# Kernel optimization log

Hardware: AMD Instinct MI355X
Metric: run time of the kernel (lower is better)

Reference implementation:

```python
import jax, jax.numpy as jnp
import numpy as np

N = 100000      # num_nodes
E = 1600000     # num_edges
IN_DIM = 6
EDGE_DIM = 2
H = 5           # heads
C = 5           # out_channels per head (hidden_dim)
D = H * C       # 25, hidden width
L = 3           # num_layers
INV_SQRT_C = np.float32(1.0 / np.sqrt(C))


def setup_inputs() -> dict:
    key = jax.random.key(0)
    ks = jax.random.split(key, 18)
    s = 0.1
    inp = {
        "x": jax.random.normal(ks[0], (N, IN_DIM), dtype=jnp.float32),
        "edge_index": jax.random.randint(ks[1], (2, E), 0, N, dtype=jnp.int64),
        "edge_attr": jax.random.normal(ks[2], (E, EDGE_DIM), dtype=jnp.float32),
        # input projection
        "Wi": jax.random.normal(ks[3], (IN_DIM, D), dtype=jnp.float32) * s,
        "bi": jnp.zeros((D,), dtype=jnp.float32),
        # per-layer TransformerConv params, stacked over layers
        "Wq": jax.random.normal(ks[4], (L, D, D), dtype=jnp.float32) * s,
        "bq": jnp.zeros((L, D), dtype=jnp.float32),
        "Wk": jax.random.normal(ks[5], (L, D, D), dtype=jnp.float32) * s,
        "bk": jnp.zeros((L, D), dtype=jnp.float32),
        "Wv": jax.random.normal(ks[6], (L, D, D), dtype=jnp.float32) * s,
        "bv": jnp.zeros((L, D), dtype=jnp.float32),
        "We": jax.random.normal(ks[7], (L, EDGE_DIM, D), dtype=jnp.float32) * s,  # lin_edge, no bias
        "Wskip": jax.random.normal(ks[8], (L, D, D), dtype=jnp.float32) * s,
        "bskip": jnp.zeros((L, D), dtype=jnp.float32),
        # output head
        "Wo": jax.random.normal(ks[9], (D, 1), dtype=jnp.float32) * s,
        "bo": jnp.zeros((1,), dtype=jnp.float32),
    }
    return inp


def _forward(x, edge_index, edge_attr, Wi, bi, Wq, bq, Wk, bk, Wv, bv, We, Wskip, bskip, Wo, bo):
    src, dst = edge_index[0], edge_index[1]
    h = x @ Wi + bi  # [N, D]
    for l in range(L):
        q = (h @ Wq[l] + bq[l]).reshape(N, H, C)
        k = (h @ Wk[l] + bk[l]).reshape(N, H, C)
        v = (h @ Wv[l] + bv[l]).reshape(N, H, C)
        e = (edge_attr @ We[l]).reshape(E, H, C)  # per-edge projection
        k_j = k[src] + e                           # [E, H, C]
        alpha = jnp.einsum('ehc,ehc->eh', q[dst], k_j) * INV_SQRT_C  # [E, H]
        # scatter-softmax over destination neighborhoods (PyG softmax)
        amax = jax.ops.segment_max(alpha, dst, num_segments=N)       # [N, H]
        ex = jnp.exp(alpha - amax[dst])
        denom = jax.ops.segment_sum(ex, dst, num_segments=N)         # [N, H]
        alpha = ex / (denom[dst] + 1e-16)
        msg = (v[src] + e) * alpha[:, :, None]                       # [E, H, C]
        out = jax.ops.segment_sum(msg, dst, num_segments=N).reshape(N, D)
        h = out + h @ Wskip[l] + bskip[l]          # root_weight skip
    return jax.nn.sigmoid(h @ Wo + bo)             # [N, 1]


def reference(x, edge_index, edge_attr, Wi, bi, Wq, bq, Wk, bk, Wv, bv, We, Wskip, bskip, Wo, bo):
    return _forward(x, edge_index, edge_attr, Wi, bi, Wq, bq, Wk, bk, Wv, bv, We, Wskip, bskip, Wo, bo)
```

## Files before the change

### kernel.cpp

```cpp
#include <hip/hip_runtime.h>
#include <hip/hip_bf16.h>
#include <math.h>

#define NN 100000
#define NE 1600000
#define IN_DIM 6
#define EDGE_DIM 2
#define HH 5
#define CC 5
#define DD 25
#define DS 32
#define QS 32
#define KVS 64
#define INV_SQRT_C 0.4472135954999579f
#define SCAN_B 256
#define NB1 ((NN + SCAN_B - 1) / SCAN_B)
#define NBUK 200
#define BUKW 500
#define CAP 10000
#define CH 8000

__device__ __forceinline__ unsigned int f2bf(float f) {
    unsigned int u = __float_as_uint(f);
    return (u + 0x7fffu + ((u >> 16) & 1u)) >> 16;
}
__device__ __forceinline__ float bflo(unsigned int u) { return __uint_as_float(u << 16); }
__device__ __forceinline__ float bfhi(unsigned int u) { return __uint_as_float(u & 0xffff0000u); }

__global__ void k_init(int* __restrict__ deg, int* __restrict__ cursor) {
    int i = blockIdx.x * 256 + threadIdx.x;
    if (i < NN) deg[i] = 0;
    if (i < NBUK) cursor[i] = i * CAP;
}

__global__ __launch_bounds__(256) void k_part(const int* __restrict__ ei,
                                              const float* __restrict__ ea,
                                              int* __restrict__ deg,
                                              int* __restrict__ cursor,
                                              uint2* __restrict__ slab) {
    __shared__ int sdst[CH];
    __shared__ int scnt[NBUK];
    __shared__ int sbase[NBUK];
    __shared__ int swp[NBUK];
    int base = blockIdx.x * CH;
    for (int i = threadIdx.x; i < NBUK; i += 256) scnt[i] = 0;
    __syncthreads();
    for (int i = threadIdx.x; i < CH; i += 256) {
        int dst = ei[NE + base + i];
        sdst[i] = dst;
        atomicAdd(&deg[dst], 1);
        atomicAdd(&scnt[dst / BUKW], 1);
    }
    __syncthreads();
    for (int i = threadIdx.x; i < NBUK; i += 256) {
        sbase[i] = atomicAdd(&cursor[i], scnt[i]);
        swp[i] = 0;
    }
    __syncthreads();
    for (int i = threadIdx.x; i < CH; i += 256) {
        int dst = sdst[i];
        int b = dst / BUKW;
        int src = ei[base + i];
        float2 eav = ((const float2*)ea)[base + i];
        int p = sbase[b] + atomicAdd(&swp[b], 1);
        uint2 r;
        r.x = (unsigned)src | ((unsigned)(dst - b * BUKW) << 17);
        r.y = f2bf(eav.x) | (f2bf(eav.y) << 16);
        slab[p] = r;
    }
}

__global__ void k_scan1(const int* __restrict__ deg, int* __restrict__ excl,
                        int* __restrict__ bsum) {
    __shared__ int s[SCAN_B];
    int i = blockIdx.x * SCAN_B + threadIdx.x;
    int v = (i < NN) ? deg[i] : 0;
    s[threadIdx.x] = v;
    __syncthreads();
    for (int off = 1; off < SCAN_B; off <<= 1) {
        int t = (threadIdx.x >= off) ? s[threadIdx.x - off] : 0;
        __syncthreads();
        s[threadIdx.x] += t;
        __syncthreads();
    }
    if (i < NN) excl[i] = s[threadIdx.x] - v;
    if (threadIdx.x == SCAN_B - 1) bsum[blockIdx.x] = s[SCAN_B - 1];
}

__global__ void k_scan2(int* __restrict__ bsum) {
    __shared__ int s[512];
    int t = threadIdx.x;
    int v = (t < NB1) ? bsum[t] : 0;
    s[t] = v;
    __syncthreads();
    for (int off = 1; off < 512; off <<= 1) {
        int u = (t >= off) ? s[t - off] : 0;
        __syncthreads();
        s[t] += u;
        __syncthreads();
    }
    if (t < NB1) bsum[t] = s[t] - v;
}

__global__ void k_scan3(const int* __restrict__ excl, const int* __restrict__ bsum,
                        int* __restrict__ rowptr) {
    int i = blockIdx.x * 256 + threadIdx.x;
    if (i < NN) rowptr[i] = excl[i] + bsum[i / SCAN_B];
    if (i == 0) rowptr[NN] = NE;
}

__global__ __launch_bounds__(256) void k_place(const int* __restrict__ cursor,
                                               const uint2* __restrict__ slab,
                                               const int* __restrict__ rowptr,
                                               uint2* __restrict__ csr) {
    __shared__ int cur[BUKW];
    int b = blockIdx.x;
    int node0 = b * BUKW;
    for (int i = threadIdx.x; i < BUKW; i += 256) cur[i] = rowptr[node0 + i];
    __syncthreads();
    int begin = b * CAP;
    int cnt = cursor[b] - begin;
    for (int i = threadIdx.x; i < cnt; i += 256) {
        uint2 r = slab[begin + i];
        int dl = (int)(r.x >> 17);
        int p = atomicAdd(&cur[dl], 1);
        uint2 o;
        o.x = r.x & 0x1FFFFu;
        o.y = r.y;
        csr[p] = o;
    }
}

__global__ void k_input_proj(const float* __restrict__ x, const float* __restrict__ Wi,
                             const float* __restrict__ bi, float* __restrict__ h) {
    __shared__ float sW[IN_DIM * DD];
    __shared__ float sb[DD];
    int t = threadIdx.x;
    if (t < IN_DIM * DD) sW[t] = Wi[t];
    if (t < DD) sb[t] = bi[t];
    __syncthreads();
    int tid = blockIdx.x * blockDim.x + t;
    int n = tid / DD, d = tid - n * DD;
    if (n >= NN) return;
    float acc = sb[d];
    const float* xr = x + n * IN_DIM;
#pragma unroll
    for (int i = 0; i < IN_DIM; i++) acc += xr[i] * sW[i * DD + d];
    h[n * DS + d] = acc;
}

__global__ void k_qkv_skip(const float* __restrict__ h,
                           const float* __restrict__ Wq, const float* __restrict__ bq,
                           const float* __restrict__ Wk, const float* __restrict__ bk,
                           const float* __restrict__ Wv, const float* __restrict__ bv,
                           const float* __restrict__ Ws, const float* __restrict__ bs,
                           __hip_bfloat16* __restrict__ q, __hip_bfloat16* __restrict__ kv,
                           float* __restrict__ hout) {
    __shared__ float sWq[DD * DD], sWk[DD * DD], sWv[DD * DD], sWs[DD * DD];
    __shared__ float sb[4 * DD];
    for (int i = threadIdx.x; i < DD * DD; i += blockDim.x) {
        sWq[i] = Wq[i]; sWk[i] = Wk[i]; sWv[i] = Wv[i]; sWs[i] = Ws[i];
    }
    if (threadIdx.x < DD) {
        sb[threadIdx.x]          = bq[threadIdx.x];
        sb[DD + threadIdx.x]     = bk[threadIdx.x];
        sb[2 * DD + threadIdx.x] = bv[threadIdx.x];
        sb[3 * DD + threadIdx.x] = bs[threadIdx.x];
    }
    __syncthreads();
    int tid = blockIdx.x * blockDim.x + threadIdx.x;
    int n = tid / DD, d = tid - n * DD;
    if (n >= NN) return;
    float aq = sb[d], ak = sb[DD + d], av = sb[2 * DD + d], asv = sb[3 * DD + d];
    const float* hr = h + (size_t)n * DS;
#pragma unroll
    for (int i = 0; i < DD; i++) {
        float hv = hr[i];
        aq  += hv * sWq[i * DD + d];
        ak  += hv * sWk[i * DD + d];
        av  += hv * sWv[i * DD + d];
        asv += hv * sWs[i * DD + d];
    }
    q[(size_t)n * QS + d] = __float2bfloat16(aq * INV_SQRT_C);
    kv[(size_t)n * KVS + d]      = __float2bfloat16(ak);
    kv[(size_t)n * KVS + 32 + d] = __float2bfloat16(av);
    hout[(size_t)n * DS + d] = asv;
}

__global__ __launch_bounds__(256) void k_edge_fused(
    const int* __restrict__ rowptr, const uint2* __restrict__ csr,
    const float* __restrict__ We, const __hip_bfloat16* __restrict__ q,
    const __hip_bfloat16* __restrict__ kv, float* __restrict__ hout) {
    __shared__ float sWe[EDGE_DIM * DD];
    if (threadIdx.x < EDGE_DIM * DD) sWe[threadIdx.x] = We[threadIdx.x];
    __syncthreads();
    int n = blockIdx.x * 32 + (threadIdx.x >> 3);
    int g = threadIdx.x & 7;
    if (n >= NN) return;
    int beg = rowptr[n], end = rowptr[n + 1];

    float qa[26];
    {
        const uint4* qr = (const uint4*)(q + (size_t)n * QS);
        uint4 q0 = qr[0], q1 = qr[1], q2 = qr[2], q3 = qr[3];
        qa[0]=bflo(q0.x); qa[1]=bfhi(q0.x); qa[2]=bflo(q0.y); qa[3]=bfhi(q0.y);
        qa[4]=bflo(q0.z); qa[5]=bfhi(q0.z); qa[6]=bflo(q0.w); qa[7]=bfhi(q0.w);
        qa[8]=bflo(q1.x); qa[9]=bfhi(q1.x); qa[10]=bflo(q1.y); qa[11]=bfhi(q1.y);
        qa[12]=bflo(q1.z); qa[13]=bfhi(q1.z); qa[14]=bflo(q1.w); qa[15]=bfhi(q1.w);
        qa[16]=bflo(q2.x); qa[17]=bfhi(q2.x); qa[18]=bflo(q2.y); qa[19]=bfhi(q2.y);
        qa[20]=bflo(q2.z); qa[21]=bfhi(q2.z); qa[22]=bflo(q2.w); qa[23]=bfhi(q2.w);
        qa[24]=bflo(q3.x);
    }
    float qwx[HH], qwy[HH];
#pragma unroll
    for (int hd = 0; hd < HH; hd++) {
        float sx = 0.0f, sy = 0.0f;
#pragma unroll
        for (int c = 0; c < CC; c++) {
            int j = hd * CC + c;
            sx += qa[j] * sWe[j];
            sy += qa[j] * sWe[DD + j];
        }
        qwx[hd] = sx; qwy[hd] = sy;
    }

    float l[HH], Sx[HH], Sy[HH], accv[DD];
#pragma unroll
    for (int hd = 0; hd < HH; hd++) { l[hd] = 0.0f; Sx[hd] = 0.0f; Sy[hd] = 0.0f; }
#pragma unroll
    for (int j = 0; j < DD; j++) accv[j] = 0.0f;

    for (int p = beg + g; p < end; p += 8) {
        uint2 rec = csr[p];
        int src = (int)rec.x;
        float eax = bflo(rec.y), eay = bfhi(rec.y);

        const uint4* kr = (const uint4*)(kv + (size_t)src * KVS);
        uint4 r0 = kr[0], r1 = kr[1], r2 = kr[2], r3 = kr[3];
        uint4 r4 = kr[4], r5 = kr[5], r6 = kr[6], r7 = kr[7];

        float kb[26];
        kb[0]=bflo(r0.x); kb[1]=bfhi(r0.x); kb[2]=bflo(r0.y); kb[3]=bfhi(r0.y);
        kb[4]=bflo(r0.z); kb[5]=bfhi(r0.z); kb[6]=bflo(r0.w); kb[7]=bfhi(r0.w);
        kb[8]=bflo(r1.x); kb[9]=bfhi(r1.x); kb[10]=bflo(r1.y); kb[11]=bfhi(r1.y);
        kb[12]=bflo(r1.z); kb[13]=bfhi(r1.z); kb[14]=bflo(r1.w); kb[15]=bfhi(r1.w);
        kb[16]=bflo(r2.x); kb[17]=bfhi(r2.x); kb[18]=bflo(r2.y); kb[19]=bfhi(r2.y);
        kb[20]=bflo(r2.z); kb[21]=bfhi(r2.z); kb[22]=bflo(r2.w); kb[23]=bfhi(r2.w);
        kb[24]=bflo(r3.x);

        float al[HH];
#pragma unroll
        for (int hd = 0; hd < HH; hd++) {
            float s = eax * qwx[hd] + eay * qwy[hd];
#pragma unroll
            for (int c = 0; c < CC; c++) {
                int j = hd * CC + c;
                s += qa[j] * kb[j];
            }
            al[hd] = __expf(s);
        }

        float vb[26];
        vb[0]=bflo(r4.x); vb[1]=bfhi(r4.x); vb[2]=bflo(r4.y); vb[3]=bfhi(r4.y);
        vb[4]=bflo(r4.z); vb[5]=bfhi(r4.z); vb[6]=bflo(r4.w); vb[7]=bfhi(r4.w);
        vb[8]=bflo(r5.x); vb[9]=bfhi(r5.x); vb[10]=bflo(r5.y); vb[11]=bfhi(r5.y);
        vb[12]=bflo(r5.z); vb[13]=bfhi(r5.z); vb[14]=bflo(r5.w); vb[15]=bfhi(r5.w);
        vb[16]=bflo(r6.x); vb[17]=bfhi(r6.x); vb[18]=bflo(r6.y); vb[19]=bfhi(r6.y);
        vb[20]=bflo(r6.z); vb[21]=bfhi(r6.z); vb[22]=bflo(r6.w); vb[23]=bfhi(r6.w);
        vb[24]=bflo(r7.x);

#pragma unroll
        for (int hd = 0; hd < HH; hd++) {
            float cf = al[hd];
            l[hd]  += cf;
            Sx[hd] += cf * eax;
            Sy[hd] += cf * eay;
#pragma unroll
            for (int c = 0; c < CC; c++) {
                int j = hd * CC + c;
                accv[j] += cf * vb[j];
            }
        }
    }

#pragma unroll
    for (int off = 1; off < 8; off <<= 1) {
#pragma unroll
        for (int hd = 0; hd < HH; hd++) {
            l[hd]  += __shfl_xor(l[hd], off, 64);
            Sx[hd] += __shfl_xor(Sx[hd], off, 64);
            Sy[hd] += __shfl_xor(Sy[hd], off, 64);
        }
#pragma unroll
        for (int j = 0; j < DD; j++) accv[j] += __shfl_xor(accv[j], off, 64);
    }

    if (g == 0) {
        float* ho = hout + (size_t)n * DS;
#pragma unroll
        for (int hd = 0; hd < HH; hd++) {
            float inv = 1.0f / (l[hd] + 1e-16f);
#pragma unroll
            for (int c = 0; c < CC; c++) {
                int j = hd * CC + c;
                ho[j] += (accv[j] + Sx[hd] * sWe[j] + Sy[hd] * sWe[DD + j]) * inv;
            }
        }
    }
}

__global__ void k_head(const float* __restrict__ h, const float* __restrict__ Wo,
                       const float* __restrict__ bo, float* __restrict__ out) {
    __shared__ float sW[DD];
    __shared__ float sb0;
    if (threadIdx.x < DD) sW[threadIdx.x] = Wo[threadIdx.x];
    if (threadIdx.x == 0) sb0 = bo[0];
    __syncthreads();
    int n = blockIdx.x * blockDim.x + threadIdx.x;
    if (n >= NN) return;
    float acc = sb0;
    const float* hr = h + (size_t)n * DS;
#pragma unroll
    for (int i = 0; i < DD; i++) acc += hr[i] * sW[i];
    out[n] = 1.0f / (1.0f + __expf(-acc));
}

extern "C" void kernel_launch(void* const* d_in, const int* in_sizes, int n_in,
                              void* d_out, int out_size, void* d_ws, size_t ws_size,
                              hipStream_t stream) {
    const float* x     = (const float*)d_in[0];
    const int*   ei    = (const int*)d_in[1];
    const float* ea    = (const float*)d_in[2];
    const float* Wi    = (const float*)d_in[3];
    const float* bi    = (const float*)d_in[4];
    const float* Wq    = (const float*)d_in[5];
    const float* bq    = (const float*)d_in[6];
    const float* Wk    = (const float*)d_in[7];
    const float* bk    = (const float*)d_in[8];
    const float* Wv    = (const float*)d_in[9];
    const float* bv    = (const float*)d_in[10];
    const float* We    = (const float*)d_in[11];
    const float* Wskip = (const float*)d_in[12];
    const float* bskip = (const float*)d_in[13];
    const float* Wo    = (const float*)d_in[14];
    const float* bo    = (const float*)d_in[15];
    float* out = (float*)d_out;
    (void)in_sizes; (void)n_in; (void)out_size; (void)ws_size;

    char* wsb = (char*)d_ws;
    size_t off = 0;
    auto alloc = [&](size_t bytes) {
        void* p = wsb + off;
        off += (bytes + 127) & ~(size_t)127;
        return p;
    };
    uint2* slab   = (uint2*)alloc((size_t)NBUK * CAP * sizeof(uint2));
    uint2* csr    = (uint2*)alloc((size_t)NE * sizeof(uint2));
    __hip_bfloat16* kvrec = (__hip_bfloat16*)alloc((size_t)NN * KVS * 2);
    __hip_bfloat16* qrec  = (__hip_bfloat16*)alloc((size_t)NN * QS * 2);
    float* hA     = (float*)alloc((size_t)NN * DS * sizeof(float));
    float* hB     = (float*)alloc((size_t)NN * DS * sizeof(float));
    int*   deg    = (int*)alloc((size_t)NN * sizeof(int));
    int*   excl   = (int*)alloc((size_t)NN * sizeof(int));
    int*   bsum   = (int*)alloc((size_t)NB1 * sizeof(int));
    int*   rowptr = (int*)alloc((size_t)(NN + 1) * sizeof(int));
    int*   cursor = (int*)alloc((size_t)NBUK * sizeof(int));

    dim3 blk(256);
    int gN  = (NN + 255) / 256;
    int gND = (NN * DD + 255) / 256;
    int gF  = NN / 32;

    k_init<<<gN, blk, 0, stream>>>(deg, cursor);
    k_part<<<NBUK, blk, 0, stream>>>(ei, ea, deg, cursor, slab);
    k_scan1<<<gN, blk, 0, stream>>>(deg, excl, bsum);
    k_scan2<<<1, dim3(512), 0, stream>>>(bsum);
    k_scan3<<<gN, blk, 0, stream>>>(excl, bsum, rowptr);
    k_place<<<NBUK, blk, 0, stream>>>(cursor, slab, rowptr, csr);

    k_input_proj<<<gND, blk, 0, stream>>>(x, Wi, bi, hA);

    float* hc = hA;
    float* hn = hB;
    for (int l = 0; l < 3; l++) {
        k_qkv_skip<<<gND, blk, 0, stream>>>(hc,
                                            Wq + (size_t)l * DD * DD, bq + (size_t)l * DD,
                                            Wk + (size_t)l * DD * DD, bk + (size_t)l * DD,
                                            Wv + (size_t)l * DD * DD, bv + (size_t)l * DD,
                                            Wskip + (size_t)l * DD * DD, bskip + (size_t)l * DD,
                                            qrec, kvrec, hn);
        k_edge_fused<<<gF, blk, 0, stream>>>(rowptr, csr,
                                             We + (size_t)l * EDGE_DIM * DD,
                                             qrec, kvrec, hn);
        float* t = hc; hc = hn; hn = t;
    }
    k_head<<<gN, blk, 0, stream>>>(hc, Wo, bo, out);
}
```

Measured before the change: 430.5 us.

## Build CSR row pointers from per-bucket histograms instead of global degree scan

```diff
diff --git a/kernel.cpp b/kernel.cpp
--- a/kernel.cpp
+++ b/kernel.cpp
@@ -13,12 +13,11 @@
 #define QS 32
 #define KVS 64
 #define INV_SQRT_C 0.4472135954999579f
-#define SCAN_B 256
-#define NB1 ((NN + SCAN_B - 1) / SCAN_B)
 #define NBUK 200
 #define BUKW 500
 #define CAP 10000
-#define CH 8000
+#define KPB 800
+#define CH (NE / KPB)
 
 __device__ __forceinline__ unsigned int f2bf(float f) {
     unsigned int u = __float_as_uint(f);
@@ -27,15 +26,13 @@
 __device__ __forceinline__ float bflo(unsigned int u) { return __uint_as_float(u << 16); }
 __device__ __forceinline__ float bfhi(unsigned int u) { return __uint_as_float(u & 0xffff0000u); }
 
-__global__ void k_init(int* __restrict__ deg, int* __restrict__ cursor) {
-    int i = blockIdx.x * 256 + threadIdx.x;
-    if (i < NN) deg[i] = 0;
+__global__ void k_init(int* __restrict__ cursor) {
+    int i = threadIdx.x;
     if (i < NBUK) cursor[i] = i * CAP;
 }
 
 __global__ __launch_bounds__(256) void k_part(const int* __restrict__ ei,
                                               const float* __restrict__ ea,
-                                              int* __restrict__ deg,
                                               int* __restrict__ cursor,
                                               uint2* __restrict__ slab) {
     __shared__ int sdst[CH];
@@ -48,7 +45,6 @@
     for (int i = threadIdx.x; i < CH; i += 256) {
         int dst = ei[NE + base + i];
         sdst[i] = dst;
-        atomicAdd(&deg[dst], 1);
         atomicAdd(&scnt[dst / BUKW], 1);
     }
     __syncthreads();
@@ -70,27 +66,45 @@
     }
 }
 
-__global__ void k_scan1(const int* __restrict__ deg, int* __restrict__ excl,
-                        int* __restrict__ bsum) {
-    __shared__ int s[SCAN_B];
-    int i = blockIdx.x * SCAN_B + threadIdx.x;
-    int v = (i < NN) ? deg[i] : 0;
-    s[threadIdx.x] = v;
-    __syncthreads();
-    for (int off = 1; off < SCAN_B; off <<= 1) {
-        int t = (threadIdx.x >= off) ? s[threadIdx.x - off] : 0;
+__global__ void k_scanB(const int* __restrict__ cursor, int* __restrict__ bucketOff,
+                        int* __restrict__ rowptr) {
+    __shared__ int s[256];
+    int t = threadIdx.x;
+    int v = (t < NBUK) ? (cursor[t] - t * CAP) : 0;
+    s[t] = v;
+    __syncthreads();
+    for (int off = 1; off < 256; off <<= 1) {
+        int u = (t >= off) ? s[t - off] : 0;
         __syncthreads();
-        s[threadIdx.x] += t;
+        s[t] += u;
         __syncthreads();
     }
-    if (i < NN) excl[i] = s[threadIdx.x] - v;
-    if (threadIdx.x == SCAN_B - 1) bsum[blockIdx.x] = s[SCAN_B - 1];
-}
-
-__global__ void k_scan2(int* __restrict__ bsum) {
+    if (t < NBUK) bucketOff[t] = s[t] - v;
+    if (t == 0) rowptr[NN] = NE;
+}
+
+__global__ __launch_bounds__(512) void k_place(const int* __restrict__ cursor,
+                                               const uint2* __restrict__ slab,
+                                               const int* __restrict__ bucketOff,
+                                               int* __restrict__ rowptr,
+                                               uint2* __restrict__ csr) {
+    __shared__ int hist[BUKW];
+    __shared__ int cur[BUKW];
     __shared__ int s[512];
+    int b = blockIdx.x;
+    int node0 = b * BUKW;
+    int begin = b * CAP;
+    int cnt = cursor[b] - begin;
+    int bOff = bucketOff[b];
+    for (int i = threadIdx.x; i < BUKW; i += 512) hist[i] = 0;
+    __syncthreads();
+    for (int i = threadIdx.x; i < cnt; i += 512) {
+        uint2 r = slab[begin + i];
+        atomicAdd(&hist[r.x >> 17], 1);
+    }
+    __syncthreads();
     int t = threadIdx.x;
-    int v = (t < NB1) ? bsum[t] : 0;
+    int v = (t < BUKW) ? hist[t] : 0;
     s[t] = v;
     __syncthreads();
     for (int off = 1; off < 512; off <<= 1) {
@@ -99,28 +113,13 @@
         s[t] += u;
         __syncthreads();
     }
-    if (t < NB1) bsum[t] = s[t] - v;
-}
-
-__global__ void k_scan3(const int* __restrict__ excl, const int* __restrict__ bsum,
-                        int* __restrict__ rowptr) {
-    int i = blockIdx.x * 256 + threadIdx.x;
-    if (i < NN) rowptr[i] = excl[i] + bsum[i / SCAN_B];
-    if (i == 0) rowptr[NN] = NE;
-}
-
-__global__ __launch_bounds__(256) void k_place(const int* __restrict__ cursor,
-                                               const uint2* __restrict__ slab,
-                                               const int* __restrict__ rowptr,
-                                               uint2* __restrict__ csr) {
-    __shared__ int cur[BUKW];
-    int b = blockIdx.x;
-    int node0 = b * BUKW;
-    for (int i = threadIdx.x; i < BUKW; i += 256) cur[i] = rowptr[node0 + i];
-    __syncthreads();
-    int begin = b * CAP;
-    int cnt = cursor[b] - begin;
-    for (int i = threadIdx.x; i < cnt; i += 256) {
+    if (t < BUKW) {
+        int o = bOff + s[t] - v;
+        rowptr[node0 + t] = o;
+        cur[t] = o;
+    }
+    __syncthreads();
+    for (int i = threadIdx.x; i < cnt; i += 512) {
         uint2 r = slab[begin + i];
         int dl = (int)(r.x >> 17);
         int p = atomicAdd(&cur[dl], 1);
@@ -360,23 +359,19 @@
     __hip_bfloat16* qrec  = (__hip_bfloat16*)alloc((size_t)NN * QS * 2);
     float* hA     = (float*)alloc((size_t)NN * DS * sizeof(float));
     float* hB     = (float*)alloc((size_t)NN * DS * sizeof(float));
-    int*   deg    = (int*)alloc((size_t)NN * sizeof(int));
-    int*   excl   = (int*)alloc((size_t)NN * sizeof(int));
-    int*   bsum   = (int*)alloc((size_t)NB1 * sizeof(int));
     int*   rowptr = (int*)alloc((size_t)(NN + 1) * sizeof(int));
     int*   cursor = (int*)alloc((size_t)NBUK * sizeof(int));
+    int*   bucketOff = (int*)alloc((size_t)NBUK * sizeof(int));
 
     dim3 blk(256);
     int gN  = (NN + 255) / 256;
     int gND = (NN * DD + 255) / 256;
     int gF  = NN / 32;
 
-    k_init<<<gN, blk, 0, stream>>>(deg, cursor);
-    k_part<<<NBUK, blk, 0, stream>>>(ei, ea, deg, cursor, slab);
-    k_scan1<<<gN, blk, 0, stream>>>(deg, excl, bsum);
-    k_scan2<<<1, dim3(512), 0, stream>>>(bsum);
-    k_scan3<<<gN, blk, 0, stream>>>(excl, bsum, rowptr);
-    k_place<<<NBUK, blk, 0, stream>>>(cursor, slab, rowptr, csr);
+    k_init<<<1, blk, 0, stream>>>(cursor);
+    k_part<<<KPB, blk, 0, stream>>>(ei, ea, cursor, slab);
+    k_scanB<<<1, blk, 0, stream>>>(cursor, bucketOff, rowptr);
+    k_place<<<NBUK, dim3(512), 0, stream>>>(cursor, slab, bucketOff, rowptr, csr);
 
     k_input_proj<<<gND, blk, 0, stream>>>(x, Wi, bi, hA);
 
```

After: 380.0 us. 11.7% less time.
